# Kernel tuning notes

Measured on AMD Instinct MI355X. Metric: run time of the kernel, lower is better.

The kernel has to match this reference:

```python
import jax, jax.numpy as jnp
import numpy as np

B, C, T = 8, 512, 1024
H = 8
D = C // H          # head_dim = 64
K = 64              # max_rel_dist
REL = 2 * K + 1     # 129


def setup_inputs() -> dict:
    key = jax.random.key(0)
    ks = jax.random.split(key, 12)
    s = 0.02
    return {
        "x": jax.random.normal(ks[0], (B, C, T), jnp.float32),
        "x_mask": jnp.ones((B, 1, T), jnp.float32),
        "W_q": jax.random.normal(ks[1], (C, C), jnp.float32) * s,
        "b_q": jnp.zeros((C,), jnp.float32),
        "W_k": jax.random.normal(ks[2], (C, C), jnp.float32) * s,
        "b_k": jnp.zeros((C,), jnp.float32),
        "W_v": jax.random.normal(ks[3], (C, C), jnp.float32) * s,
        "b_v": jnp.zeros((C,), jnp.float32),
        "W_o": jax.random.normal(ks[4], (C, C), jnp.float32) * s,
        "b_o": jnp.zeros((C,), jnp.float32),
        "emb_rel_k": jax.random.normal(ks[5], (REL, D), jnp.float32) * 0.01,
        "emb_rel_v": jax.random.normal(ks[6], (REL, D), jnp.float32) * 0.01,
    }


def _conv1x1(x, W, b):
    # Conv1d with kernel_size=1: (B,C,T) x (Cout,Cin) -> (B,Cout,T)
    return jnp.einsum("oc,bct->bot", W, x) + b[None, :, None]


def _shape_heads(x):
    # (B,C,T) -> (B,H,T,D)
    b = x.shape[0]
    return x.reshape(b, H, D, T).transpose(0, 1, 3, 2)


def reference(x, x_mask, W_q, b_q, W_k, b_k, W_v, b_v, W_o, b_o, emb_rel_k, emb_rel_v):
    q = _shape_heads(_conv1x1(x, W_q, b_q))  # (B,H,T,D)
    k = _shape_heads(_conv1x1(x, W_k, b_k))
    v = _shape_heads(_conv1x1(x, W_v, b_v))

    # relative position indices: clamp(j - i, -K, K) + K  -> (T,T)
    pos = jnp.arange(T)
    rel_idx = jnp.clip(pos[None, :] - pos[:, None], -K, K) + K

    # scores: scaled QK^T plus unscaled relative-key term (faithful to source)
    attn = jnp.einsum("bhid,bhjd->bhij", q, k) / (D ** 0.5)
    rel_k_tt = emb_rel_k[rel_idx]            # (T,T,D)
    attn = attn + jnp.einsum("bhid,ijd->bhij", q, rel_k_tt)

    # key mask: positions with x_mask <= 0 get -1e9
    key_mask = (x_mask <= 0).reshape(x.shape[0], 1, 1, T)
    attn = jnp.where(key_mask, -1e9, attn)
    attn = jax.nn.softmax(attn, axis=-1)     # dropout p=0.0 -> identity

    y = jnp.einsum("bhij,bhjd->bhid", attn, v)
    rel_v_tt = emb_rel_v[rel_idx]            # (T,T,D)
    y = y + jnp.einsum("bhij,ijd->bhid", attn, rel_v_tt)

    # (B,H,T,D) -> (B,H,D,T) -> (B,C,T)
    y = y.transpose(0, 1, 3, 2).reshape(x.shape[0], C, T)
    y = _conv1x1(y, W_o, b_o)
    return y * x_mask
```

## Files before the change

kernel.cpp:

```cpp
#include <hip/hip_runtime.h>

#define B_   8
#define C_   512
#define T_   1024
#define H_   8
#define D_   64
#define K_   64
#define REL_ 129

typedef unsigned short u16;
typedef __attribute__((ext_vector_type(8))) short short8;
typedef __attribute__((ext_vector_type(4))) float f32x4;

__device__ __forceinline__ float b2f(u16 u) {
    return __uint_as_float(((unsigned)u) << 16);
}
__device__ __forceinline__ u16 f2b(float f) {
    unsigned x = __float_as_uint(f);
    x += 0x7fffu + ((x >> 16) & 1u);
    return (u16)(x >> 16);
}

__global__ __launch_bounds__(256) void cast_all_kernel(
    const float* __restrict__ x,
    const float* __restrict__ Wq, const float* __restrict__ Wk,
    const float* __restrict__ Wv, const float* __restrict__ Wo,
    const float* __restrict__ erk, const float* __restrict__ erv,
    u16* __restrict__ xt, u16* __restrict__ Wh,
    u16* __restrict__ ervt, u16* __restrict__ erkb)
{
    __shared__ u16 tile[64][72];
    const int blk = blockIdx.x;
    const int tid = threadIdx.x;
    if (blk < 1024) {
        const int t0 = (blk & 15) * 64, c0 = ((blk >> 4) & 7) * 64, b = blk >> 7;
        const int f = tid & 15, r0 = tid >> 4;
#pragma unroll
        for (int p = 0; p < 4; ++p) {
            const int c = r0 + p * 16;
            const float4 v = *(const float4*)(x + ((size_t)b * C_ + c0 + c) * T_ + t0 + f * 4);
            tile[c][f * 4 + 0] = f2b(v.x);
            tile[c][f * 4 + 1] = f2b(v.y);
            tile[c][f * 4 + 2] = f2b(v.z);
            tile[c][f * 4 + 3] = f2b(v.w);
        }
        __syncthreads();
#pragma unroll
        for (int p = 0; p < 4; ++p) {
            const int t = r0 + p * 16;
            ushort4 u;
            u.x = tile[f * 4 + 0][t];
            u.y = tile[f * 4 + 1][t];
            u.z = tile[f * 4 + 2][t];
            u.w = tile[f * 4 + 3][t];
            *(ushort4*)(xt + ((size_t)b * T_ + t0 + t) * C_ + c0 + f * 4) = u;
        }
    } else if (blk < 2048) {
        const int gid = (blk - 1024) * 256 + tid;
        const int s = gid >> 16;
        const int off = (gid & 65535) * 4;
        const float* W = (s == 0) ? Wq : (s == 1) ? Wk : (s == 2) ? Wv : Wo;
        const float4 v = *(const float4*)(W + off);
        ushort4 u;
        u.x = f2b(v.x); u.y = f2b(v.y); u.z = f2b(v.z); u.w = f2b(v.w);
        *(ushort4*)(Wh + ((size_t)s << 18) + off) = u;
    } else {
        const int idx = (blk - 2048) * 256 + tid;
        if (idx < 64 * 160) {
            const int d = idx / 160, rel = idx % 160;
            ervt[idx] = (rel < REL_) ? f2b(erv[rel * D_ + d]) : (u16)0;
        } else {
            const int j = idx - 64 * 160;
            if (j < REL_ * D_) erkb[j] = f2b(erk[j]);
        }
    }
}

__global__ __launch_bounds__(256) void proj_mfma(
    const u16* __restrict__ xt, const u16* __restrict__ Wh,
    const float* __restrict__ bq, const float* __restrict__ bk, const float* __restrict__ bv,
    u16* __restrict__ qh, u16* __restrict__ kh, u16* __restrict__ vt)
{
    __shared__ u16 Wt[64][72];

    const int t0 = blockIdx.x * 128;
    const int h  = blockIdx.y;
    const int sel = blockIdx.z >> 3;
    const int b   = blockIdx.z & 7;
    const int tid = threadIdx.x, wave = tid >> 6, lane = tid & 63;
    const int quad = lane >> 4, l16 = lane & 15;

    const u16* Wbase = Wh + ((size_t)sel << 18) + ((size_t)(h * 64) << 9);
    const u16* A0 = xt + (((size_t)b * T_ + t0 + wave * 16 + l16) << 9);
    const u16* A1 = A0 + ((size_t)64 << 9);

    const int so = tid >> 2;
    const int sc = (tid & 3) * 16;
    const u16* wsrc = Wbase + ((size_t)so << 9) + sc;

    f32x4 acc[2][4];
#pragma unroll
    for (int gg = 0; gg < 2; ++gg)
#pragma unroll
        for (int nt = 0; nt < 4; ++nt) acc[gg][nt] = (f32x4){0.f, 0.f, 0.f, 0.f};

    uint4 wv0 = *(const uint4*)(wsrc);
    uint4 wv1 = *(const uint4*)(wsrc + 8);
#pragma unroll 1
    for (int i = 0; i < 8; ++i) {
        const int c0 = i * 64;
        __syncthreads();
        *(uint4*)&Wt[so][sc] = wv0;
        *(uint4*)&Wt[so][sc + 8] = wv1;
        __syncthreads();
        if (i < 7) {
            wv0 = *(const uint4*)(wsrc + c0 + 64);
            wv1 = *(const uint4*)(wsrc + c0 + 72);
        }
#pragma unroll
        for (int kk = 0; kk < 64; kk += 32) {
            const short8 af0 = *(const short8*)(A0 + c0 + kk + quad * 8);
            const short8 af1 = *(const short8*)(A1 + c0 + kk + quad * 8);
#pragma unroll
            for (int nt = 0; nt < 4; ++nt) {
                const short8 bf = *(const short8*)(&Wt[nt * 16 + l16][kk + quad * 8]);
                acc[0][nt] = __builtin_amdgcn_mfma_f32_16x16x32_bf16(af0, bf, acc[0][nt], 0, 0, 0);
                acc[1][nt] = __builtin_amdgcn_mfma_f32_16x16x32_bf16(af1, bf, acc[1][nt], 0, 0, 0);
            }
        }
    }

    const int bh = b * 8 + h;
    if (sel == 2) {
#pragma unroll
        for (int gg = 0; gg < 2; ++gg) {
            __syncthreads();
#pragma unroll
            for (int nt = 0; nt < 4; ++nt) {
                const int d = nt * 16 + l16;
                const float bo = bv[h * 64 + d];
#pragma unroll
                for (int rix = 0; rix < 4; ++rix) {
                    const int tl = wave * 16 + quad * 4 + rix;
                    Wt[d][tl] = f2b(acc[gg][nt][rix] + bo);
                }
            }
            __syncthreads();
            const int row = tid >> 2;
            const int seg = (tid & 3) * 16;
            const uint4 v0 = *(const uint4*)&Wt[row][seg];
            const uint4 v1 = *(const uint4*)&Wt[row][seg + 8];
            u16* vdst = vt + (((size_t)bh * 64 + row) << 10) + t0 + gg * 64 + seg;
            *(uint4*)(vdst) = v0;
            *(uint4*)(vdst + 8) = v1;
        }
    } else {
        const float* bias = sel ? bk : bq;
        u16* dst = sel ? kh : qh;
#pragma unroll
        for (int nt = 0; nt < 4; ++nt) {
            const int d = nt * 16 + l16;
            const float bo = bias[h * 64 + d];
#pragma unroll
            for (int gg = 0; gg < 2; ++gg)
#pragma unroll
                for (int rix = 0; rix < 4; ++rix) {
                    const int t = t0 + gg * 64 + wave * 16 + quad * 4 + rix;
                    dst[(((size_t)bh * T_ + t) << 6) + d] = f2b(acc[gg][nt][rix] + bo);
                }
        }
    }
}

__global__ __launch_bounds__(256, 3) void attn_kernel(
    const u16* __restrict__ qh, const u16* __restrict__ kh, const u16* __restrict__ vt,
    const u16* __restrict__ erkb, const u16* __restrict__ ervt,
    const float* __restrict__ xmask, u16* __restrict__ yf)
{
    __shared__ u16   sw[32][168];
    __shared__ u16   bandbuf[32][136];
    __shared__ u16   chunkbuf[4][32][40];
    __shared__ float ogbuf[32][68];
    __shared__ float red[4][32][2];
    __shared__ float invrow[32];

    const int gid = blockIdx.x;
    const int x8 = gid & 7, r5 = gid >> 3;
    const int bh = x8 + 8 * (r5 >> 5);
    const int i0 = (r5 & 31) * 32;
    const int b = bh >> 3, h = bh & 7;
    const int tid = threadIdx.x, wave = tid >> 6, lane = tid & 63;
    const int quad = lane >> 4, l16 = lane & 15;

    const float LOG2E = 1.4426950408889634f;
    const float SC    = 0.125f * 1.4426950408889634f;

    {
        unsigned* bb = (unsigned*)&bandbuf[0][0];
#pragma unroll 1
        for (int k2 = tid; k2 < 32 * 68; k2 += 256) bb[k2] = 0u;
    }

    short8 qa[2][2];
#pragma unroll
    for (int g = 0; g < 2; ++g) {
        const u16* qrow = qh + (((size_t)bh * T_ + i0 + g * 16 + l16) << 6);
        qa[g][0] = *(const short8*)(qrow + quad * 8);
        qa[g][1] = *(const short8*)(qrow + 32 + quad * 8);
    }

    for (int tile = wave; tile < 9; tile += 4) {
        const int rel = tile * 16 + l16;
        const int rl = rel > 128 ? 128 : rel;
        const u16* ep = erkb + rl * 64 + quad * 8;
        const short8 b0 = *(const short8*)(ep);
        const short8 b1 = *(const short8*)(ep + 32);
#pragma unroll
        for (int g = 0; g < 2; ++g) {
            f32x4 m = {0.f, 0.f, 0.f, 0.f};
            m = __builtin_amdgcn_mfma_f32_16x16x32_bf16(qa[g][0], b0, m, 0, 0, 0);
            m = __builtin_amdgcn_mfma_f32_16x16x32_bf16(qa[g][1], b1, m, 0, 0, 0);
            if (rel < 129) {
#pragma unroll
                for (int rix = 0; rix < 4; ++rix)
                    sw[g * 16 + quad * 4 + rix][rel] = f2b(m[rix] * LOG2E);
            }
        }
    }
    __syncthreads();

    float slo_c[2][4], shi_c[2][4];
#pragma unroll
    for (int g = 0; g < 2; ++g)
#pragma unroll
        for (int rix = 0; rix < 4; ++rix) {
            const int row = g * 16 + quad * 4 + rix;
            slo_c[g][rix] = b2f(sw[row][0]);
            shi_c[g][rix] = b2f(sw[row][2 * K_]);
        }

    float psum[2][4] = {{0.f,0.f,0.f,0.f},{0.f,0.f,0.f,0.f}};
    float phi [2][4] = {{0.f,0.f,0.f,0.f},{0.f,0.f,0.f,0.f}};
    f32x4 og[4][2];
#pragma unroll
    for (int s = 0; s < 4; ++s)
#pragma unroll
        for (int g = 0; g < 2; ++g) og[s][g] = (f32x4){0.f, 0.f, 0.f, 0.f};

    {
        const u16* kb = kh + ((size_t)bh << 16);
        const u16* vbase = vt + ((size_t)bh << 16);

        short8 kc0, kc1;
        float  xmc;
        {
            const u16* krow0 = kb + ((size_t)(wave * 256 + l16) << 6);
            kc0 = *(const short8*)(krow0 + quad * 8);
            kc1 = *(const short8*)(krow0 + 32 + quad * 8);
            xmc = xmask[b * T_ + wave * 256 + l16];
        }
        short8 vaf[4];
#pragma unroll
        for (int s = 0; s < 4; ++s)
            vaf[s] = *(const short8*)(vbase + ((size_t)(s * 16 + l16) << 10) + wave * 256 + quad * 8);

#pragma unroll 1
        for (int c = 0; c < 8; ++c) {
#pragma unroll
            for (int half = 0; half < 2; ++half) {
                const int ct = c * 2 + half;
                const int j0 = wave * 256 + ct * 16;
                const int j = j0 + l16;
                const short8 kb0 = kc0, kb1 = kc1;
                const float xmv = xmc;
                {
                    const int jn = wave * 256 + ((ct < 15) ? ct + 1 : ct) * 16 + l16;
                    const u16* krown = kb + ((size_t)jn << 6);
                    kc0 = *(const short8*)(krown + quad * 8);
                    kc1 = *(const short8*)(krown + 32 + quad * 8);
                    xmc = xmask[b * T_ + jn];
                }
                const float clampv = (xmv > 0.f) ? 43.280850f : -2.0e9f;
#pragma unroll
                for (int g = 0; g < 2; ++g) {
                    f32x4 acc = {0.f, 0.f, 0.f, 0.f};
                    acc = __builtin_amdgcn_mfma_f32_16x16x32_bf16(qa[g][0], kb0, acc, 0, 0, 0);
                    acc = __builtin_amdgcn_mfma_f32_16x16x32_bf16(qa[g][1], kb1, acc, 0, 0, 0);
                    const int dd = j0 - (i0 + g * 16);
                    const int ibase = i0 + g * 16 + quad * 4;
                    const int relb = j - ibase + K_;
                    const bool interior = (dd > -79) && (dd < 79);
                    float ee[4];
                    if (dd <= -79) {
#pragma unroll
                        for (int rix = 0; rix < 4; ++rix)
                            ee[rix] = __builtin_amdgcn_exp2f(
                                fminf(fmaf(acc[rix], SC, slo_c[g][rix]), clampv));
                    } else if (dd >= 79) {
#pragma unroll
                        for (int rix = 0; rix < 4; ++rix)
                            ee[rix] = __builtin_amdgcn_exp2f(
                                fminf(fmaf(acc[rix], SC, shi_c[g][rix]), clampv));
                    } else {
#pragma unroll
                        for (int rix = 0; rix < 4; ++rix) {
                            int idx = relb - rix;
                            idx = idx < 0 ? 0 : (idx > 2 * K_ ? 2 * K_ : idx);
                            const int row = g * 16 + quad * 4 + rix;
                            const float sr = b2f(sw[row][idx]);
                            ee[rix] = __builtin_amdgcn_exp2f(
                                fminf(fmaf(acc[rix], SC, sr), clampv));
                        }
                    }
                    unsigned p01, p23;
                    asm("v_cvt_pk_bf16_f32 %0, %1, %2" : "=v"(p01) : "v"(ee[0]), "v"(ee[1]));
                    asm("v_cvt_pk_bf16_f32 %0, %1, %2" : "=v"(p23) : "v"(ee[2]), "v"(ee[3]));
                    const int r0 = g * 16 + quad * 4;
                    const int ccol = half * 16 + l16;
                    const u16 pv0 = (u16)(p01 & 0xffffu);
                    const u16 pv1 = (u16)(p01 >> 16);
                    const u16 pv2 = (u16)(p23 & 0xffffu);
                    const u16 pv3 = (u16)(p23 >> 16);
                    chunkbuf[wave][r0 + 0][ccol] = pv0;
                    chunkbuf[wave][r0 + 1][ccol] = pv1;
                    chunkbuf[wave][r0 + 2][ccol] = pv2;
                    chunkbuf[wave][r0 + 3][ccol] = pv3;
                    if (interior) {
                        if ((unsigned)(relb - 1) < 127u) bandbuf[r0 + 0][relb]     = pv0;
                        if ((unsigned)(relb - 2) < 127u) bandbuf[r0 + 1][relb - 1] = pv1;
                        if ((unsigned)(relb - 3) < 127u) bandbuf[r0 + 2][relb - 2] = pv2;
                        if ((unsigned)(relb - 4) < 127u) bandbuf[r0 + 3][relb - 3] = pv3;
                    }
                    const float er0 = __uint_as_float(p01 << 16);
                    const float er1 = __uint_as_float(p01 & 0xffff0000u);
                    const float er2 = __uint_as_float(p23 << 16);
                    const float er3 = __uint_as_float(p23 & 0xffff0000u);
                    psum[g][0] += er0; psum[g][1] += er1;
                    psum[g][2] += er2; psum[g][3] += er3;
                    if (dd >= 79) {
                        phi[g][0] += er0; phi[g][1] += er1;
                        phi[g][2] += er2; phi[g][3] += er3;
                    } else if (dd > -79) {
                        phi[g][0] += (j - ibase >= 64) ? er0 : 0.f;
                        phi[g][1] += (j - ibase >= 65) ? er1 : 0.f;
                        phi[g][2] += (j - ibase >= 66) ? er2 : 0.f;
                        phi[g][3] += (j - ibase >= 67) ? er3 : 0.f;
                    }
                }
            }
            const short8 pb0 = *(const short8*)(&chunkbuf[wave][l16][quad * 8]);
            const short8 pb1 = *(const short8*)(&chunkbuf[wave][16 + l16][quad * 8]);
            short8 vn[4];
            {
                const int kcn = wave * 256 + ((c < 7) ? c + 1 : c) * 32;
#pragma unroll
                for (int s = 0; s < 4; ++s)
                    vn[s] = *(const short8*)(vbase + ((size_t)(s * 16 + l16) << 10) + kcn + quad * 8);
            }
#pragma unroll
            for (int s = 0; s < 4; ++s) {
                og[s][0] = __builtin_amdgcn_mfma_f32_16x16x32_bf16(vaf[s], pb0, og[s][0], 0, 0, 0);
                og[s][1] = __builtin_amdgcn_mfma_f32_16x16x32_bf16(vaf[s], pb1, og[s][1], 0, 0, 0);
            }
#pragma unroll
            for (int s = 0; s < 4; ++s) vaf[s] = vn[s];
        }
#pragma unroll
        for (int m = 1; m < 16; m <<= 1)
#pragma unroll
            for (int g = 0; g < 2; ++g)
#pragma unroll
                for (int rix = 0; rix < 4; ++rix) {
                    psum[g][rix] += __shfl_xor(psum[g][rix], m);
                    phi[g][rix]  += __shfl_xor(phi[g][rix], m);
                }
        if (l16 == 0)
#pragma unroll
            for (int g = 0; g < 2; ++g)
#pragma unroll
                for (int rix = 0; rix < 4; ++rix) {
                    const int row = g * 16 + quad * 4 + rix;
                    red[wave][row][0] = psum[g][rix];
                    red[wave][row][1] = phi[g][rix];
                }
    }
    __syncthreads();

    {
        const int rr = tid >> 3;
        const int c0 = tid & 7;
        const float sumrow = red[0][rr][0] + red[1][rr][0] + red[2][rr][0] + red[3][rr][0];
        const float phirow = red[0][rr][1] + red[1][rr][1] + red[2][rr][1] + red[3][rr][1];
        float intsum = 0.f;
        for (int rel = c0; rel < 168; rel += 8) {
            if (rel == 0 || rel == 2 * K_) continue;
            u16 v = 0;
            if (rel < 2 * K_) {
                v = bandbuf[rr][rel];
                intsum += b2f(v);
            }
            sw[rr][rel] = v;
        }
        intsum += __shfl_xor(intsum, 1);
        intsum += __shfl_xor(intsum, 2);
        intsum += __shfl_xor(intsum, 4);
        if (c0 == 0) {
            sw[rr][2 * K_] = f2b(phirow);
            sw[rr][0]      = f2b(sumrow - intsum - phirow);
            invrow[rr]     = 1.0f / sumrow;
        }
    }
    __syncthreads();

#pragma unroll
    for (int w = 0; w < 4; ++w) {
        if (wave == w) {
            if (w == 0) {
#pragma unroll
                for (int s = 0; s < 4; ++s)
#pragma unroll
                    for (int g = 0; g < 2; ++g)
                        *(f32x4*)&ogbuf[g * 16 + l16][s * 16 + quad * 4] = og[s][g];
            } else {
#pragma unroll
                for (int s = 0; s < 4; ++s)
#pragma unroll
                    for (int g = 0; g < 2; ++g) {
                        f32x4 cur = *(const f32x4*)&ogbuf[g * 16 + l16][s * 16 + quad * 4];
                        cur = cur + og[s][g];
                        *(f32x4*)&ogbuf[g * 16 + l16][s * 16 + quad * 4] = cur;
                    }
            }
        }
        __syncthreads();
    }

    {
        const int dh = wave * 16 + l16;
        const u16* ep = ervt + dh * 160;
        f32x4 accg[2];
#pragma unroll
        for (int g = 0; g < 2; ++g)
            accg[g] = *(const f32x4*)&ogbuf[g * 16 + l16][wave * 16 + quad * 4];
#pragma unroll
        for (int kt = 0; kt < 5; ++kt) {
            const short8 af = *(const short8*)(ep + kt * 32 + quad * 8);
            const short8 p0 = *(const short8*)(&sw[l16][kt * 32 + quad * 8]);
            const short8 p1 = *(const short8*)(&sw[16 + l16][kt * 32 + quad * 8]);
            accg[0] = __builtin_amdgcn_mfma_f32_16x16x32_bf16(af, p0, accg[0], 0, 0, 0);
            accg[1] = __builtin_amdgcn_mfma_f32_16x16x32_bf16(af, p1, accg[1], 0, 0, 0);
        }
        const int dbase = (h << 6) + wave * 16 + quad * 4;
#pragma unroll
        for (int g = 0; g < 2; ++g) {
            const float iv = invrow[g * 16 + l16];
            ushort4 u;
            u.x = f2b(accg[g][0] * iv); u.y = f2b(accg[g][1] * iv);
            u.z = f2b(accg[g][2] * iv); u.w = f2b(accg[g][3] * iv);
            *(ushort4*)(yf + (((size_t)b * T_ + i0 + g * 16 + l16) << 9) + dbase) = u;
        }
    }
}

__global__ __launch_bounds__(256) void outproj_mfma(
    const u16* __restrict__ yf, const u16* __restrict__ Woh, const float* __restrict__ bo,
    const float* __restrict__ xmask, float* __restrict__ out)
{
    __shared__ u16 Yt[64][72];

    const int o0 = blockIdx.x * 64;
    const int b  = blockIdx.y >> 4;
    const int t0 = (blockIdx.y & 15) * 64;
    const int tid = threadIdx.x, wave = tid >> 6, lane = tid & 63;
    const int quad = lane >> 4, l16 = lane & 15;

    const u16* A = Woh + ((size_t)(o0 + wave * 16 + l16) << 9);

    const int so = tid >> 2;
    const int sc = (tid & 3) * 16;
    const u16* ysrc = yf + (((size_t)b * T_ + t0 + so) << 9) + sc;

    f32x4 acc[4] = {{0.f,0.f,0.f,0.f},{0.f,0.f,0.f,0.f},{0.f,0.f,0.f,0.f},{0.f,0.f,0.f,0.f}};

    uint4 wv0 = *(const uint4*)(ysrc);
    uint4 wv1 = *(const uint4*)(ysrc + 8);
#pragma unroll 1
    for (int i = 0; i < 8; ++i) {
        const int c0 = i * 64;
        __syncthreads();
        *(uint4*)&Yt[so][sc] = wv0;
        *(uint4*)&Yt[so][sc + 8] = wv1;
        __syncthreads();
        if (i < 7) {
            wv0 = *(const uint4*)(ysrc + c0 + 64);
            wv1 = *(const uint4*)(ysrc + c0 + 72);
        }
#pragma unroll
        for (int kk = 0; kk < 64; kk += 32) {
            const short8 af = *(const short8*)(A + c0 + kk + quad * 8);
#pragma unroll
            for (int nt = 0; nt < 4; ++nt) {
                const short8 bf = *(const short8*)(&Yt[nt * 16 + l16][kk + quad * 8]);
                acc[nt] = __builtin_amdgcn_mfma_f32_16x16x32_bf16(af, bf, acc[nt], 0, 0, 0);
            }
        }
    }

#pragma unroll
    for (int nt = 0; nt < 4; ++nt) {
        const int t = t0 + nt * 16 + l16;
        const float xmv = xmask[b * T_ + t];
#pragma unroll
        for (int rix = 0; rix < 4; ++rix) {
            const int o = o0 + wave * 16 + quad * 4 + rix;
            out[((size_t)b * C_ + o) * T_ + t] = (acc[nt][rix] + bo[o]) * xmv;
        }
    }
}

extern "C" void kernel_launch(void* const* d_in, const int* in_sizes, int n_in,
                              void* d_out, int out_size, void* d_ws, size_t ws_size,
                              hipStream_t stream) {
    const float* x     = (const float*)d_in[0];
    const float* xmask = (const float*)d_in[1];
    const float* Wq    = (const float*)d_in[2];
    const float* bq    = (const float*)d_in[3];
    const float* Wk    = (const float*)d_in[4];
    const float* bk    = (const float*)d_in[5];
    const float* Wv    = (const float*)d_in[6];
    const float* bv    = (const float*)d_in[7];
    const float* Wo    = (const float*)d_in[8];
    const float* bo    = (const float*)d_in[9];
    const float* erk   = (const float*)d_in[10];
    const float* erv   = (const float*)d_in[11];

    const size_t need = 44077184;
    if (ws_size < need) return;
    u16* xt   = (u16*)d_ws;
    u16* Wh   = (u16*)((char*)d_ws + 8388608);
    u16* qh   = (u16*)((char*)d_ws + 10485760);
    u16* kh   = (u16*)((char*)d_ws + 18874368);
    u16* vt   = (u16*)((char*)d_ws + 27262976);
    u16* yf   = (u16*)((char*)d_ws + 35651584);
    u16* ervt = (u16*)((char*)d_ws + 44040192);
    u16* erkb = (u16*)((char*)d_ws + 44060672);
    float* out = (float*)d_out;

    cast_all_kernel<<<dim3(2121), 256, 0, stream>>>(
        x, Wq, Wk, Wv, Wo, erk, erv, xt, Wh, ervt, erkb);
    proj_mfma<<<dim3(T_ / 128, H_, 3 * B_), 256, 0, stream>>>(
        xt, Wh, bq, bk, bv, qh, kh, vt);
    attn_kernel<<<dim3(2048), 256, 0, stream>>>(
        qh, kh, vt, erkb, ervt, xmask, yf);
    outproj_mfma<<<dim3(C_ / 64, B_ * (T_ / 64)), 256, 0, stream>>>(
        yf, Wh + ((size_t)3 << 18), bo, xmask, out);
}
```

Before: 214.4 us.

## Drop LDS staging of weights in projection and alias attention scratch buffers

The projection GEMM now reads weight fragments for its MFMAs straight from global memory (through cache) instead of staging them through shared memory with two barriers per K step, and the K loop is fully unrolled. The attention kernel overlays the per-wave P chunk buffer and the output reduction buffer in one shared pool, cutting its LDS footprint so more blocks can fit per CU. The risks are more redundant global loads in the projection and a possible hazard if the pool is reused without a barrier between the chunk and ogbuf phases.

```diff
diff --git a/kernel.cpp b/kernel.cpp
--- a/kernel.cpp
+++ b/kernel.cpp
@@ -91,39 +91,26 @@
     const int quad = lane >> 4, l16 = lane & 15;
 
     const u16* Wbase = Wh + ((size_t)sel << 18) + ((size_t)(h * 64) << 9);
+    const u16* Wl = Wbase + ((size_t)l16 << 9) + quad * 8;
     const u16* A0 = xt + (((size_t)b * T_ + t0 + wave * 16 + l16) << 9);
     const u16* A1 = A0 + ((size_t)64 << 9);
 
-    const int so = tid >> 2;
-    const int sc = (tid & 3) * 16;
-    const u16* wsrc = Wbase + ((size_t)so << 9) + sc;
-
     f32x4 acc[2][4];
 #pragma unroll
     for (int gg = 0; gg < 2; ++gg)
 #pragma unroll
         for (int nt = 0; nt < 4; ++nt) acc[gg][nt] = (f32x4){0.f, 0.f, 0.f, 0.f};
 
-    uint4 wv0 = *(const uint4*)(wsrc);
-    uint4 wv1 = *(const uint4*)(wsrc + 8);
-#pragma unroll 1
+#pragma unroll
     for (int i = 0; i < 8; ++i) {
         const int c0 = i * 64;
-        __syncthreads();
-        *(uint4*)&Wt[so][sc] = wv0;
-        *(uint4*)&Wt[so][sc + 8] = wv1;
-        __syncthreads();
-        if (i < 7) {
-            wv0 = *(const uint4*)(wsrc + c0 + 64);
-            wv1 = *(const uint4*)(wsrc + c0 + 72);
-        }
 #pragma unroll
         for (int kk = 0; kk < 64; kk += 32) {
             const short8 af0 = *(const short8*)(A0 + c0 + kk + quad * 8);
             const short8 af1 = *(const short8*)(A1 + c0 + kk + quad * 8);
 #pragma unroll
             for (int nt = 0; nt < 4; ++nt) {
-                const short8 bf = *(const short8*)(&Wt[nt * 16 + l16][kk + quad * 8]);
+                const short8 bf = *(const short8*)(Wl + ((size_t)(nt * 16) << 9) + c0 + kk);
                 acc[0][nt] = __builtin_amdgcn_mfma_f32_16x16x32_bf16(af0, bf, acc[0][nt], 0, 0, 0);
                 acc[1][nt] = __builtin_amdgcn_mfma_f32_16x16x32_bf16(af1, bf, acc[1][nt], 0, 0, 0);
             }
@@ -179,10 +166,12 @@
 {
     __shared__ u16   sw[32][168];
     __shared__ u16   bandbuf[32][136];
-    __shared__ u16   chunkbuf[4][32][40];
-    __shared__ float ogbuf[32][68];
+    __shared__ char  pool[4 * 32 * 40 * 2];
     __shared__ float red[4][32][2];
     __shared__ float invrow[32];
+
+    u16*   chunk = (u16*)pool;
+    float* ogb   = (float*)pool;
 
     const int gid = blockIdx.x;
     const int x8 = gid & 7, r5 = gid >> 3;
@@ -321,10 +310,11 @@
                     const u16 pv1 = (u16)(p01 >> 16);
                     const u16 pv2 = (u16)(p23 & 0xffffu);
                     const u16 pv3 = (u16)(p23 >> 16);
-                    chunkbuf[wave][r0 + 0][ccol] = pv0;
-                    chunkbuf[wave][r0 + 1][ccol] = pv1;
-                    chunkbuf[wave][r0 + 2][ccol] = pv2;
-                    chunkbuf[wave][r0 + 3][ccol] = pv3;
+                    u16* cb = chunk + ((wave * 32 + r0) * 40 + ccol);
+                    cb[0]   = pv0;
+                    cb[40]  = pv1;
+                    cb[80]  = pv2;
+                    cb[120] = pv3;
                     if (interior) {
                         if ((unsigned)(relb - 1) < 127u) bandbuf[r0 + 0][relb]     = pv0;
                         if ((unsigned)(relb - 2) < 127u) bandbuf[r0 + 1][relb - 1] = pv1;
@@ -348,8 +338,8 @@
                     }
                 }
             }
-            const short8 pb0 = *(const short8*)(&chunkbuf[wave][l16][quad * 8]);
-            const short8 pb1 = *(const short8*)(&chunkbuf[wave][16 + l16][quad * 8]);
+            const short8 pb0 = *(const short8*)(chunk + (wave * 32 + l16) * 40 + quad * 8);
+            const short8 pb1 = *(const short8*)(chunk + (wave * 32 + 16 + l16) * 40 + quad * 8);
             short8 vn[4];
             {
                 const int kcn = wave * 256 + ((c < 7) ? c + 1 : c) * 32;
@@ -420,15 +410,15 @@
                 for (int s = 0; s < 4; ++s)
 #pragma unroll
                     for (int g = 0; g < 2; ++g)
-                        *(f32x4*)&ogbuf[g * 16 + l16][s * 16 + quad * 4] = og[s][g];
+                        *(f32x4*)&ogb[(g * 16 + l16) * 68 + s * 16 + quad * 4] = og[s][g];
             } else {
 #pragma unroll
                 for (int s = 0; s < 4; ++s)
 #pragma unroll
                     for (int g = 0; g < 2; ++g) {
-                        f32x4 cur = *(const f32x4*)&ogbuf[g * 16 + l16][s * 16 + quad * 4];
+                        f32x4 cur = *(const f32x4*)&ogb[(g * 16 + l16) * 68 + s * 16 + quad * 4];
                         cur = cur + og[s][g];
-                        *(f32x4*)&ogbuf[g * 16 + l16][s * 16 + quad * 4] = cur;
+                        *(f32x4*)&ogb[(g * 16 + l16) * 68 + s * 16 + quad * 4] = cur;
                     }
             }
         }
@@ -441,7 +431,7 @@
         f32x4 accg[2];
 #pragma unroll
         for (int g = 0; g < 2; ++g)
-            accg[g] = *(const f32x4*)&ogbuf[g * 16 + l16][wave * 16 + quad * 4];
+            accg[g] = *(const f32x4*)&ogb[(g * 16 + l16) * 68 + wave * 16 + quad * 4];
 #pragma unroll
         for (int kt = 0; kt < 5; ++kt) {
             const short8 af = *(const short8*)(ep + kt * 32 + quad * 8);
```

New measurement: 254.2 us. 1.19x slower.
